# Kernel optimization log

Measured on AMD Instinct MI355X. Metric: run time of the kernel, lower is better.

The kernel has to match this reference:

```python
import jax, jax.numpy as jnp
import numpy as np

DT = 1e-3   # timestep (s)
DH = 10.0   # grid spacing (m)


def setup_inputs() -> dict:
    key = jax.random.key(0)
    k1, k2, k3, k4 = jax.random.split(key, 4)
    B, NT, NZ, NX, NREC = 8, 256, 256, 256, 64
    x = jax.random.normal(k1, (B, NT), dtype=jnp.float32)            # source wavelets
    vp = 1500.0 + 2000.0 * jax.random.uniform(k2, (NZ, NX), dtype=jnp.float32)
    src_loc = jax.random.randint(k3, (B, 2), 4, NZ - 4, dtype=jnp.int32)        # (z,x) per shot
    rec_loc = jax.random.randint(k4, (B, NREC, 2), 4, NZ - 4, dtype=jnp.int32)  # (z,x) per rec
    return {"x": x, "vp": vp, "src_loc": src_loc, "rec_loc": rec_loc}


def reference(x, vp, src_loc, rec_loc):
    """Acoustic 2nd-order leapfrog FD time-stepping (WaveRNN pattern):
    per step: stencil update -> source scatter-inject -> receiver gather.
    Returns receiver traces (B, NT, NREC)."""
    B, NT = x.shape
    nz, nx = vp.shape
    c2dt2 = (vp * vp) * jnp.float32(DT * DT)   # (nz, nx), broadcast over batch
    inv_dh2 = jnp.float32(1.0 / (DH * DH))
    bidx = jnp.arange(B)
    sz, sx = src_loc[:, 0], src_loc[:, 1]
    rz, rx = rec_loc[..., 0], rec_loc[..., 1]

    def laplacian(h):  # 5-point stencil, zero (Dirichlet) boundaries
        interior = (h[:, 2:, 1:-1] + h[:, :-2, 1:-1]
                    + h[:, 1:-1, 2:] + h[:, 1:-1, :-2]
                    - 4.0 * h[:, 1:-1, 1:-1]) * inv_dh2
        return jnp.zeros_like(h).at[:, 1:-1, 1:-1].set(interior)

    def step(carry, wav_t):
        h1, h2 = carry                              # fields at t, t-1
        hn = 2.0 * h1 - h2 + c2dt2 * laplacian(h1)  # leapfrog update
        hn = hn.at[bidx, sz, sx].add(jnp.float32(DT * DT) * wav_t)  # source inject
        rec = hn[bidx[:, None], rz, rx]             # receiver gather (B, NREC)
        return (hn, h1), rec

    h0 = jnp.zeros((B, nz, nx), dtype=x.dtype)
    _, recs = jax.lax.scan(step, (h0, h0), x.T)     # recs: (NT, B, NREC)
    return jnp.transpose(recs, (1, 0, 2))           # (B, NT, NREC)
```

## Files before the change

### kernel.cpp

```cpp
#include <hip/hip_runtime.h>

typedef float v4f __attribute__((ext_vector_type(4)));

namespace {
constexpr int B_     = 8;
constexpr int NT_    = 256;
constexpr int NX_    = 256;
constexpr int NREC_  = 64;
constexpr int PIECES = 16;
constexpr int IROWS  = 16;
constexpr int G      = 16;
constexpr int ROUNDS = NT_ / G;
constexpr int NB     = (IROWS + 2 * G) / 4;
constexpr int NTHR   = NB * 64;
constexpr int NBLK   = B_ * PIECES;
constexpr float DT2  = 1e-6f;
constexpr float KLAP = 1e-8f;
constexpr size_t FLAGS_BYTES = 4096;
constexpr int RCAP = 6;
}

__device__ __forceinline__ float dpp_shr1(float v) {
    return __int_as_float(__builtin_amdgcn_update_dpp(
        0, __float_as_int(v), 0x138 , 0xF, 0xF, true));
}
__device__ __forceinline__ float dpp_shl1(float v) {
    return __int_as_float(__builtin_amdgcn_update_dpp(
        0, __float_as_int(v), 0x130 , 0xF, 0xF, true));
}

__device__ __forceinline__ void store_v4_sys(float* p, v4f v) {
    asm volatile("global_store_dwordx4 %0, %1, off sc0 sc1"
                 :: "v"(p), "v"(v) : "memory");
}
__device__ __forceinline__ v4f load_v4_sys(const float* p) {
    v4f r;
    asm volatile("global_load_dwordx4 %0, %1, off sc0 sc1"
                 : "=v"(r) : "v"(p) : "memory");
    return r;
}

extern "C" __global__
__attribute__((amdgpu_flat_work_group_size(NTHR, NTHR), amdgpu_waves_per_eu(4, 4)))
void wave_reg_kernel(const float* __restrict__ x,
                     const float* __restrict__ vp,
                     const int* __restrict__ src_loc,
                     const int* __restrict__ rec_loc,
                     float* __restrict__ out,
                     int* __restrict__ flags,
                     float* __restrict__ gbuf)
{
    __shared__ float pub[2][2][NB][256];
    __shared__ float wav[NT_];
    __shared__ float recbuf[G][NREC_];
    __shared__ unsigned char recown[NREC_];

    const int bid  = blockIdx.x;
    const int b    = bid & 7;
    const int p    = bid >> 3;
    const int blk  = b * PIECES + p;
    const int tid  = threadIdx.x;
    const int band = tid >> 6;
    const int lane = tid & 63;
    const int c0   = lane << 2;
    const int grt  = p * IROWS - G + (band << 2);

    const int cut = (band < 4) ? ((band << 2) + 3)
                  : ((band < 8) ? G : (47 - (band << 2)));

    if (tid < NT_) wav[tid] = x[b * NT_ + tid];
    if (tid < NREC_) {
        int rz = rec_loc[(b * NREC_ + tid) * 2 + 0];
        recown[tid] = (rz >= p * IROWS && rz < p * IROWS + IROWS) ? 1 : 0;
    }

    v4f cf[4], cf2[4];
#pragma unroll
    for (int i = 0; i < 4; ++i) {
        int gr = grt + i;
        int crow = gr < 0 ? 0 : (gr > 255 ? 255 : gr);
        bool rowok = (gr >= 1) && (gr <= 254);
        v4f vv = *(const v4f*)&vp[crow * NX_ + c0];
        float cc[4];
#pragma unroll
        for (int k = 0; k < 4; ++k) {
            int col = c0 + k;
            float vk = (k == 0) ? vv.x : (k == 1) ? vv.y : (k == 2) ? vv.z : vv.w;
            cc[k] = (rowok && col >= 1 && col <= 254) ? vk * vk * KLAP : 0.f;
        }
        cf[i].x = cc[0]; cf[i].y = cc[1]; cf[i].z = cc[2]; cf[i].w = cc[3];
        cf2[i].x = 2.f - 4.f * cc[0]; cf2[i].y = 2.f - 4.f * cc[1];
        cf2[i].z = 2.f - 4.f * cc[2]; cf2[i].w = 2.f - 4.f * cc[3];
    }

    const int sz = src_loc[b * 2 + 0], sx = src_loc[b * 2 + 1];
    const int si = sz - grt;
    const int sj = sx - c0;
    const bool has_src = ((unsigned)si < 4u) && ((unsigned)sj < 4u);
    const bool wave_has_src = __any(has_src);

    int rs[RCAP]; int rcnt = 0;
#pragma unroll 1
    for (int r = 0; r < NREC_; ++r) {
        int rz = rec_loc[(b * NREC_ + r) * 2 + 0];
        int rx = rec_loc[(b * NREC_ + r) * 2 + 1];
        int i = rz - grt, j = rx - c0;
        if (rz >= p * IROWS && rz < p * IROWS + IROWS &&
            (unsigned)i < 4u && (unsigned)j < 4u) {
            if (rcnt < RCAP) rs[rcnt] = (r << 4) | (i << 2) | j;
            ++rcnt;
        }
    }
    if (rcnt > RCAP) rcnt = RCAP;
    const bool wave_has_rec = __any(rcnt > 0);
    float* outb = out + (size_t)b * NT_ * NREC_;

    v4f A[4], Bv[4];
    {
        v4f z = {0.f, 0.f, 0.f, 0.f};
#pragma unroll
        for (int i = 0; i < 4; ++i) { A[i] = z; Bv[i] = z; }
    }

    auto gptr = [&](int e, int bk, int lvl, int rr) -> float* {
        return gbuf + ((((size_t)(e & 1) * NBLK + bk) * 2 + lvl) * 16 + rr) * 256;
    };

    auto step = [&](v4f (&C)[4], v4f (&P)[4], int t, int par) {
        const int k = (t & (G - 1)) + 1;
        if (k <= cut + 1) {
            *(v4f*)&pub[par][0][band][c0] = C[0];
            *(v4f*)&pub[par][1][band][c0] = C[3];
        }
        __syncthreads();
        if (k > cut) return;
        v4f nn, ss;
        if (band > 0)      nn = *(const v4f*)&pub[par][1][band - 1][c0];
        else               { nn.x = 0.f; nn.y = 0.f; nn.z = 0.f; nn.w = 0.f; }
        if (band < NB - 1) ss = *(const v4f*)&pub[par][0][band + 1][c0];
        else               { ss.x = 0.f; ss.y = 0.f; ss.z = 0.f; ss.w = 0.f; }
#pragma unroll
        for (int i = 0; i < 4; ++i) {
            v4f n = (i == 0) ? nn : C[i - 1];
            v4f s = (i == 3) ? ss : C[i + 1];
            float wv = dpp_shr1(C[i].w);
            float ev = dpp_shl1(C[i].x);
            v4f hn;
            { float sm = (n.x + s.x) + (wv     + C[i].y);
              hn.x = fmaf(cf[i].x, sm, fmaf(cf2[i].x, C[i].x, -P[i].x)); }
            { float sm = (n.y + s.y) + (C[i].x + C[i].z);
              hn.y = fmaf(cf[i].y, sm, fmaf(cf2[i].y, C[i].y, -P[i].y)); }
            { float sm = (n.z + s.z) + (C[i].y + C[i].w);
              hn.z = fmaf(cf[i].z, sm, fmaf(cf2[i].z, C[i].z, -P[i].z)); }
            { float sm = (n.w + s.w) + (C[i].z + ev);
              hn.w = fmaf(cf[i].w, sm, fmaf(cf2[i].w, C[i].w, -P[i].w)); }
            P[i] = hn;
        }
        if (wave_has_src) {
            const float sv = DT2 * wav[t];
#pragma unroll
            for (int i = 0; i < 4; ++i) {
                if (has_src && si == i) {
                    if      (sj == 0) P[i].x += sv;
                    else if (sj == 1) P[i].y += sv;
                    else if (sj == 2) P[i].z += sv;
                    else              P[i].w += sv;
                }
            }
        }
        if (wave_has_rec) {
#pragma unroll
            for (int kk = 0; kk < RCAP; ++kk) {
                if (rcnt > kk) {
                    int pk = rs[kk];
                    int i = (pk >> 2) & 3, j = pk & 3, r = pk >> 4;
                    v4f t01 = (i & 1) ? P[1] : P[0];
                    v4f t23 = (i & 1) ? P[3] : P[2];
                    v4f rw  = (i & 2) ? t23 : t01;
                    float c01 = (j & 1) ? rw.y : rw.x;
                    float c23 = (j & 1) ? rw.w : rw.z;
                    recbuf[t & (G - 1)][r] = (j & 2) ? c23 : c01;
                }
            }
        }
    };

    auto publish_prev = [&](int e) {
        if (band >= 4 && band < 8) {
            int rr0 = (band - 4) << 2;
#pragma unroll
            for (int i = 0; i < 4; ++i)
                store_v4_sys(&gptr(e, blk, 1, rr0 + i)[c0], Bv[i]);
        }
    };

    auto exchange = [&](int e) {
        if (band >= 4 && band < 8) {
            int rr0 = (band - 4) << 2;
#pragma unroll
            for (int i = 0; i < 4; ++i)
                store_v4_sys(&gptr(e, blk, 0, rr0 + i)[c0], A[i]);
        }
        __syncthreads();
        if (tid == 0)
            __hip_atomic_store(&flags[blk], e + 1, __ATOMIC_RELAXED,
                               __HIP_MEMORY_SCOPE_SYSTEM);
        if (band < 4 && p > 0) {
            if (lane == 0)
                while (__hip_atomic_load(&flags[blk - 1], __ATOMIC_RELAXED,
                                         __HIP_MEMORY_SCOPE_SYSTEM) < e + 1)
                    __builtin_amdgcn_s_sleep(1);
            int rr0 = band << 2;
#pragma unroll
            for (int i = 0; i < 4; ++i) {
                A[i]  = load_v4_sys(&gptr(e, blk - 1, 0, rr0 + i)[c0]);
                Bv[i] = load_v4_sys(&gptr(e, blk - 1, 1, rr0 + i)[c0]);
            }
        }
        if (band >= 8 && p < PIECES - 1) {
            if (lane == 0)
                while (__hip_atomic_load(&flags[blk + 1], __ATOMIC_RELAXED,
                                         __HIP_MEMORY_SCOPE_SYSTEM) < e + 1)
                    __builtin_amdgcn_s_sleep(1);
            int rr0 = (band - 8) << 2;
#pragma unroll
            for (int i = 0; i < 4; ++i) {
                A[i]  = load_v4_sys(&gptr(e, blk + 1, 0, rr0 + i)[c0]);
                Bv[i] = load_v4_sys(&gptr(e, blk + 1, 1, rr0 + i)[c0]);
            }
        }
        asm volatile("s_waitcnt vmcnt(0)" ::: "memory");
        __builtin_amdgcn_sched_barrier(0);
        __syncthreads();
    };

    int t = 0;
#pragma unroll 1
    for (int e = 0; e < ROUNDS; ++e) {
#pragma unroll 1
        for (int s = 0; s < G; s += 2) {
            step(A, Bv, t, 0);
            if (s == G - 2 && e < ROUNDS - 1)
                publish_prev(e);
            step(Bv, A, t + 1, 1);
            t += 2;
        }
        __syncthreads();
#pragma unroll 1
        for (int idx = tid; idx < G * NREC_; idx += NTHR) {
            int s = idx >> 6, r = idx & 63;
            if (recown[r]) outb[(e * G + s) * NREC_ + r] = recbuf[s][r];
        }
        if (e < ROUNDS - 1) exchange(e);
    }
}

extern "C" void kernel_launch(void* const* d_in, const int* in_sizes, int n_in,
                              void* d_out, int out_size, void* d_ws, size_t ws_size,
                              hipStream_t stream) {
    const float* x   = (const float*)d_in[0];
    const float* vp  = (const float*)d_in[1];
    const int*   src = (const int*)d_in[2];
    const int*   rec = (const int*)d_in[3];
    float*       o   = (float*)d_out;
    int*   flags = (int*)d_ws;
    float* gbuf  = (float*)((char*)d_ws + FLAGS_BYTES);
    (void)hipMemsetAsync(d_ws, 0, FLAGS_BYTES, stream);
    hipLaunchKernelGGL(wave_reg_kernel, dim3(NBLK), dim3(NTHR), 0, stream,
                       x, vp, src, rec, o, flags, gbuf);
}
```

Before: 286.0 us.

## Split domain into thinner pieces with deeper temporal halo and multi-hop exchange

Each shot's grid is now split into 32 pieces of 8 interior rows instead of 16 pieces of 16, and the temporal block grows to 24 steps per round (a final round of 16), with a 24-row halo on each side. Halo rows are fetched from up to three neighbouring pieces per round, so there are fewer global exchange rounds and twice as many blocks to fill the GPU. In exchange, each block does much more redundant halo computation relative to its useful interior rows, and the multi-hop flag waits couple more blocks together at each exchange.

```diff
diff --git a/kernel.cpp b/kernel.cpp
--- a/kernel.cpp
+++ b/kernel.cpp
@@ -7,11 +7,12 @@
 constexpr int NT_    = 256;
 constexpr int NX_    = 256;
 constexpr int NREC_  = 64;
-constexpr int PIECES = 16;
-constexpr int IROWS  = 16;
-constexpr int G      = 16;
-constexpr int ROUNDS = NT_ / G;
-constexpr int NB     = (IROWS + 2 * G) / 4;
+constexpr int PIECES = 32;
+constexpr int IROWS  = 8;
+constexpr int GN     = 24;
+constexpr int GL     = 16;
+constexpr int NRND   = 11;
+constexpr int NB     = 14;
 constexpr int NTHR   = NB * 64;
 constexpr int NBLK   = B_ * PIECES;
 constexpr float DT2  = 1e-6f;
@@ -52,7 +53,7 @@
 {
     __shared__ float pub[2][2][NB][256];
     __shared__ float wav[NT_];
-    __shared__ float recbuf[G][NREC_];
+    __shared__ float recbuf[GN][NREC_];
     __shared__ unsigned char recown[NREC_];
 
     const int bid  = blockIdx.x;
@@ -63,10 +64,10 @@
     const int band = tid >> 6;
     const int lane = tid & 63;
     const int c0   = lane << 2;
-    const int grt  = p * IROWS - G + (band << 2);
-
-    const int cut = (band < 4) ? ((band << 2) + 3)
-                  : ((band < 8) ? G : (47 - (band << 2)));
+    const int grt  = p * IROWS - GN + (band << 2);
+
+    const int cutbase = (band < 6) ? ((band << 2) + 3)
+                      : ((band < 8) ? GN : (55 - (band << 2)));
 
     if (tid < NT_) wav[tid] = x[b * NT_ + tid];
     if (tid < NREC_) {
@@ -123,17 +124,16 @@
     }
 
     auto gptr = [&](int e, int bk, int lvl, int rr) -> float* {
-        return gbuf + ((((size_t)(e & 1) * NBLK + bk) * 2 + lvl) * 16 + rr) * 256;
-    };
-
-    auto step = [&](v4f (&C)[4], v4f (&P)[4], int t, int par) {
-        const int k = (t & (G - 1)) + 1;
-        if (k <= cut + 1) {
+        return gbuf + ((((size_t)(e & 1) * NBLK + bk) * 2 + lvl) * 8 + rr) * 256;
+    };
+
+    auto step = [&](v4f (&C)[4], v4f (&P)[4], int t, int par, int k, int cutr) {
+        if (k <= cutr + 1) {
             *(v4f*)&pub[par][0][band][c0] = C[0];
             *(v4f*)&pub[par][1][band][c0] = C[3];
         }
         __syncthreads();
-        if (k > cut) return;
+        if (k > cutr) return;
         v4f nn, ss;
         if (band > 0)      nn = *(const v4f*)&pub[par][1][band - 1][c0];
         else               { nn.x = 0.f; nn.y = 0.f; nn.z = 0.f; nn.w = 0.f; }
@@ -179,15 +179,15 @@
                     v4f rw  = (i & 2) ? t23 : t01;
                     float c01 = (j & 1) ? rw.y : rw.x;
                     float c23 = (j & 1) ? rw.w : rw.z;
-                    recbuf[t & (G - 1)][r] = (j & 2) ? c23 : c01;
+                    recbuf[k - 1][r] = (j & 2) ? c23 : c01;
                 }
             }
         }
     };
 
     auto publish_prev = [&](int e) {
-        if (band >= 4 && band < 8) {
-            int rr0 = (band - 4) << 2;
+        if (band == 6 || band == 7) {
+            int rr0 = (band - 6) << 2;
 #pragma unroll
             for (int i = 0; i < 4; ++i)
                 store_v4_sys(&gptr(e, blk, 1, rr0 + i)[c0], Bv[i]);
@@ -195,8 +195,8 @@
     };
 
     auto exchange = [&](int e) {
-        if (band >= 4 && band < 8) {
-            int rr0 = (band - 4) << 2;
+        if (band == 6 || band == 7) {
+            int rr0 = (band - 6) << 2;
 #pragma unroll
             for (int i = 0; i < 4; ++i)
                 store_v4_sys(&gptr(e, blk, 0, rr0 + i)[c0], A[i]);
@@ -205,28 +205,27 @@
         if (tid == 0)
             __hip_atomic_store(&flags[blk], e + 1, __ATOMIC_RELAXED,
                                __HIP_MEMORY_SCOPE_SYSTEM);
-        if (band < 4 && p > 0) {
-            if (lane == 0)
-                while (__hip_atomic_load(&flags[blk - 1], __ATOMIC_RELAXED,
-                                         __HIP_MEMORY_SCOPE_SYSTEM) < e + 1)
-                    __builtin_amdgcn_s_sleep(1);
-            int rr0 = band << 2;
-#pragma unroll
-            for (int i = 0; i < 4; ++i) {
-                A[i]  = load_v4_sys(&gptr(e, blk - 1, 0, rr0 + i)[c0]);
-                Bv[i] = load_v4_sys(&gptr(e, blk - 1, 1, rr0 + i)[c0]);
-            }
-        }
-        if (band >= 8 && p < PIECES - 1) {
-            if (lane == 0)
-                while (__hip_atomic_load(&flags[blk + 1], __ATOMIC_RELAXED,
-                                         __HIP_MEMORY_SCOPE_SYSTEM) < e + 1)
-                    __builtin_amdgcn_s_sleep(1);
-            int rr0 = (band - 8) << 2;
-#pragma unroll
-            for (int i = 0; i < 4; ++i) {
-                A[i]  = load_v4_sys(&gptr(e, blk + 1, 0, rr0 + i)[c0]);
-                Bv[i] = load_v4_sys(&gptr(e, blk + 1, 1, rr0 + i)[c0]);
+        {
+            int hop = 0;
+            if      (band < 2)  hop = -3;
+            else if (band < 4)  hop = -2;
+            else if (band < 6)  hop = -1;
+            else if (band >= 12) hop = 3;
+            else if (band >= 10) hop = 2;
+            else if (band >= 8)  hop = 1;
+            const int srcp = p + hop;
+            if (hop != 0 && srcp >= 0 && srcp < PIECES) {
+                const int srcblk = blk + hop;
+                if (lane == 0)
+                    while (__hip_atomic_load(&flags[srcblk], __ATOMIC_RELAXED,
+                                             __HIP_MEMORY_SCOPE_SYSTEM) < e + 1)
+                        __builtin_amdgcn_s_sleep(1);
+                int rr0 = (band & 1) << 2;
+#pragma unroll
+                for (int i = 0; i < 4; ++i) {
+                    A[i]  = load_v4_sys(&gptr(e, srcblk, 0, rr0 + i)[c0]);
+                    Bv[i] = load_v4_sys(&gptr(e, srcblk, 1, rr0 + i)[c0]);
+                }
             }
         }
         asm volatile("s_waitcnt vmcnt(0)" ::: "memory");
@@ -236,22 +235,24 @@
 
     int t = 0;
 #pragma unroll 1
-    for (int e = 0; e < ROUNDS; ++e) {
-#pragma unroll 1
-        for (int s = 0; s < G; s += 2) {
-            step(A, Bv, t, 0);
-            if (s == G - 2 && e < ROUNDS - 1)
+    for (int e = 0; e < NRND; ++e) {
+        const int Gr   = (e < NRND - 1) ? GN : GL;
+        const int cutr = cutbase < Gr ? cutbase : Gr;
+#pragma unroll 1
+        for (int k = 1; k <= Gr; k += 2) {
+            step(A, Bv, t, 0, k, cutr);
+            if (k == Gr - 1 && e < NRND - 1)
                 publish_prev(e);
-            step(Bv, A, t + 1, 1);
+            step(Bv, A, t + 1, 1, k + 1, cutr);
             t += 2;
         }
         __syncthreads();
 #pragma unroll 1
-        for (int idx = tid; idx < G * NREC_; idx += NTHR) {
+        for (int idx = tid; idx < Gr * NREC_; idx += NTHR) {
             int s = idx >> 6, r = idx & 63;
-            if (recown[r]) outb[(e * G + s) * NREC_ + r] = recbuf[s][r];
-        }
-        if (e < ROUNDS - 1) exchange(e);
+            if (recown[r]) outb[(t - Gr + s) * NREC_ + r] = recbuf[s][r];
+        }
+        if (e < NRND - 1) exchange(e);
     }
 }
 
```

Measured after the change: 288.2 us. About the same (+0.8%).
